# Optimization experiments

Measured on AMD Instinct MI355X. Metric: run time of the kernel, lower is better.

## Reference

```python
import jax, jax.numpy as jnp
import numpy as np

B, S, D_IN, H, G, HD = 1, 2048, 2048, 32, 8, 128
GS = H // G  # group_size = 4
D_OUT = H * HD  # 4096
EPS = 1e-6


def _rmsnorm(x, scale):
    # qwen3-compatible: compute in fp32 over last dim
    xf = x.astype(jnp.float32)
    var = jnp.mean(xf * xf, axis=-1, keepdims=True)
    return (xf * jax.lax.rsqrt(var + EPS) * scale).astype(x.dtype)


def _apply_rope(x, cos, sin):
    # x: [b, h, s, d]; cos/sin: [s, d]
    d2 = x.shape[-1] // 2
    x1, x2 = x[..., :d2], x[..., d2:]
    rotated = jnp.concatenate([-x2, x1], axis=-1)
    return (x * cos[None, None] + rotated * sin[None, None]).astype(x.dtype)


def setup_inputs() -> dict:
    key = jax.random.key(0)
    ks = jax.random.split(key, 8)
    x = jax.random.normal(ks[0], (B, S, D_IN), jnp.float32)
    mask = jnp.triu(jnp.ones((S, S), bool), k=1)  # causal: True = masked
    # RoPE tables [S, HD]
    inv_freq = 1.0 / (10000.0 ** (jnp.arange(0, HD, 2, dtype=jnp.float32) / HD))
    ang = jnp.arange(S, dtype=jnp.float32)[:, None] * inv_freq[None, :]
    ang = jnp.concatenate([ang, ang], axis=-1)
    cos, sin = jnp.cos(ang), jnp.sin(ang)
    std = 0.02
    Wq = jax.random.normal(ks[1], (D_IN, D_OUT), jnp.float32) * std
    Wk = jax.random.normal(ks[2], (D_IN, G * HD), jnp.float32) * std
    Wv = jax.random.normal(ks[3], (D_IN, G * HD), jnp.float32) * std
    Wo = jax.random.normal(ks[4], (D_OUT, D_IN), jnp.float32) * std
    q_scale = jnp.ones((HD,), jnp.float32)
    k_scale = jnp.ones((HD,), jnp.float32)
    return {"x": x, "mask": mask, "cos": cos, "sin": sin,
            "Wq": Wq, "Wk": Wk, "Wv": Wv, "Wo": Wo,
            "q_scale": q_scale, "k_scale": k_scale}


def reference(x, mask, cos, sin, Wq, Wk, Wv, Wo, q_scale, k_scale):
    b, s, _ = x.shape
    q = (x @ Wq).reshape(b, s, H, HD).transpose(0, 2, 1, 3)   # [b,H,s,hd]
    k = (x @ Wk).reshape(b, s, G, HD).transpose(0, 2, 1, 3)   # [b,G,s,hd]
    v = (x @ Wv).reshape(b, s, G, HD).transpose(0, 2, 1, 3)   # [b,G,s,hd]
    q = _rmsnorm(q, q_scale)
    k = _rmsnorm(k, k_scale)
    q = _apply_rope(q, cos[:s], sin[:s])
    k = _apply_rope(k, cos[:s], sin[:s])
    next_k, next_v = k, v  # cache (num_kv_groups heads)
    # GQA via broadcasting instead of repeat_interleave (same math)
    qg = q.reshape(b, G, GS, s, HD)
    scores = jnp.einsum('bgrsd,bgtd->bgrst', qg, k)           # [b,G,gs,s,s]
    scores = jnp.where(mask[None, None, None], -jnp.inf, scores)
    attn = jax.nn.softmax(scores / np.sqrt(HD).astype(np.float32), axis=-1)
    ctx = jnp.einsum('bgrst,bgtd->bgrsd', attn, v)            # [b,G,gs,s,hd]
    ctx = ctx.reshape(b, H, s, HD).transpose(0, 2, 1, 3).reshape(b, s, D_OUT)
    out = ctx @ Wo
    return out, next_k, next_v
```

## Files before the change

### kernel.cpp

```cpp
#include <hip/hip_runtime.h>

typedef unsigned short ushort_t;
typedef short short8 __attribute__((ext_vector_type(8)));
typedef float floatx4 __attribute__((ext_vector_type(4)));

#define S_LEN 2048
#define DIN   2048
#define NH    32
#define NG    8
#define HDIM  128
#define DOUT  4096
#define DKV   1024
#define QLD   6144

__device__ __forceinline__ float b2f(ushort_t u) {
  union { float f; unsigned u; } t; t.u = ((unsigned)u) << 16; return t.f;
}
__device__ __forceinline__ ushort_t f2b(float f) {
  union { float f; unsigned u; } t; t.f = f;
  unsigned v = t.u;
  v += 0x7FFFu + ((v >> 16) & 1u);
  return (ushort_t)(v >> 16);
}

__device__ __forceinline__ void glds16(const ushort_t* g, ushort_t* l) {
  __builtin_amdgcn_global_load_lds((const __attribute__((address_space(1))) void*)g,
                                   (__attribute__((address_space(3))) void*)l, 16, 0, 0);
}

__global__ __launch_bounds__(256) void tcastW(const float* __restrict__ Wq,
                                              const float* __restrict__ Wk,
                                              const float* __restrict__ Wv,
                                              ushort_t* __restrict__ Wt) {
  __shared__ float t[32][33];
  const int x = blockIdx.x;
  const float* W; int N, sx, drow;
  if (x < 128)      { W = Wq; N = DOUT; sx = x * 32;         drow = x * 32; }
  else if (x < 160) { W = Wk; N = DKV;  sx = (x - 128) * 32; drow = 4096 + (x - 128) * 32; }
  else              { W = Wv; N = DKV;  sx = (x - 160) * 32; drow = 5120 + (x - 160) * 32; }
  const int by = blockIdx.y * 32;
  const int tx = threadIdx.x & 31;
  const int ty = threadIdx.x >> 5;
#pragma unroll
  for (int i = 0; i < 32; i += 8)
    t[ty + i][tx] = W[(size_t)(by + ty + i) * N + sx + tx];
  __syncthreads();
#pragma unroll
  for (int i = 0; i < 32; i += 8)
    Wt[(size_t)(drow + ty + i) * DIN + by + tx] = f2b(t[tx][ty + i]);
}

__global__ __launch_bounds__(256) void tcast(const float* __restrict__ W,
                                             ushort_t* __restrict__ Wt,
                                             int N, int ldt) {
  __shared__ float t[32][33];
  const int bx = blockIdx.x * 32;
  const int by = blockIdx.y * 32;
  const int tx = threadIdx.x & 31;
  const int ty = threadIdx.x >> 5;
#pragma unroll
  for (int i = 0; i < 32; i += 8)
    t[ty + i][tx] = W[(size_t)(by + ty + i) * N + bx + tx];
  __syncthreads();
#pragma unroll
  for (int i = 0; i < 32; i += 8)
    Wt[(size_t)(bx + ty + i) * ldt + by + tx] = f2b(t[tx][ty + i]);
}

__global__ __launch_bounds__(256) void castx(const float* __restrict__ x,
                                             ushort_t* __restrict__ xb) {
  const size_t i = ((size_t)blockIdx.x * 256 + threadIdx.x) * 4;
  float4 v = *(const float4*)&x[i];
  union { int2 p; ushort_t s[4]; } w;
  w.s[0] = f2b(v.x); w.s[1] = f2b(v.y); w.s[2] = f2b(v.z); w.s[3] = f2b(v.w);
  *(int2*)&xb[i] = w.p;
}

template <int CF32, int BM>
__global__ __launch_bounds__(256) void gemm_glds(const ushort_t* __restrict__ A, int lda,
                                                 const ushort_t* __restrict__ Bt, int ldb,
                                                 void* __restrict__ Cp, int ldc, int K) {
  constexpr int MI = BM / 32;
  __shared__ __align__(16) ushort_t As[3][BM * 32];
  __shared__ __align__(16) ushort_t Bs[3][4096];
  const int tid  = threadIdx.x;
  const int m0   = blockIdx.y * BM;
  const int n0   = blockIdx.x * 128;
  const int wave = tid >> 6, lane = tid & 63;
  const int lrow = lane & 15, quad = lane >> 4;
  const int wm = (wave >> 1) * (BM / 2), wn = (wave & 1) * 64;

  floatx4 acc[MI][4];
#pragma unroll
  for (int mi = 0; mi < MI; mi++)
#pragma unroll
    for (int ni = 0; ni < 4; ni++)
#pragma unroll
      for (int j = 0; j < 4; j++) acc[mi][ni][j] = 0.0f;

  const int sc = ((tid & 3) ^ ((tid >> 3) & 3)) * 8;
  const ushort_t* ag0 = A + (size_t)(m0 + (tid >> 2)) * lda + sc;
  const ushort_t* ag1 = ag0 + (size_t)64 * lda;
  const ushort_t* bg0 = Bt + (size_t)(n0 + (tid >> 2)) * ldb + sc;
  const ushort_t* bg1 = bg0 + (size_t)64 * ldb;
  const int so = wave * 512;

  auto stage = [&](int k0, ushort_t* aB, ushort_t* bB) {
    glds16(ag0 + k0, aB + so);
    if constexpr (BM == 128) glds16(ag1 + k0, aB + 2048 + so);
    glds16(bg0 + k0, bB + so);
    glds16(bg1 + k0, bB + 2048 + so);
  };

  const int rq = (quad ^ ((lrow >> 1) & 3)) * 8;

  stage(0,  As[0], Bs[0]);
  stage(32, As[1], Bs[1]);
  stage(64, As[2], Bs[2]);

  ushort_t *a_cur = As[0], *a_n1 = As[1], *a_n2 = As[2];
  ushort_t *b_cur = Bs[0], *b_n1 = Bs[1], *b_n2 = Bs[2];

  const int NT = K >> 5;
  for (int t = 0; t < NT; t++) {
    if (t + 2 < NT) {
      if constexpr (BM == 128) asm volatile("s_waitcnt vmcnt(8)" ::: "memory");
      else                     asm volatile("s_waitcnt vmcnt(6)" ::: "memory");
    } else if (t + 1 < NT) {
      if constexpr (BM == 128) asm volatile("s_waitcnt vmcnt(4)" ::: "memory");
      else                     asm volatile("s_waitcnt vmcnt(3)" ::: "memory");
    } else {
      asm volatile("s_waitcnt vmcnt(0)" ::: "memory");
    }
    __builtin_amdgcn_s_barrier();

    short8 af[MI], bfr[4];
#pragma unroll
    for (int mi = 0; mi < MI; mi++)
      af[mi] = *(const short8*)&a_cur[(wm + mi * 16 + lrow) * 32 + rq];
#pragma unroll
    for (int ni = 0; ni < 4; ni++)
      bfr[ni] = *(const short8*)&b_cur[(wn + ni * 16 + lrow) * 32 + rq];
    asm volatile("s_waitcnt lgkmcnt(0)" ::: "memory");
    __builtin_amdgcn_s_barrier();

    if (t + 3 < NT) stage((t + 3) << 5, a_cur, b_cur);

    __builtin_amdgcn_s_setprio(1);
#pragma unroll
    for (int mi = 0; mi < MI; mi++)
#pragma unroll
      for (int ni = 0; ni < 4; ni++)
        acc[mi][ni] = __builtin_amdgcn_mfma_f32_16x16x32_bf16(af[mi], bfr[ni], acc[mi][ni], 0, 0, 0);
    __builtin_amdgcn_s_setprio(0);

    ushort_t* ta = a_cur; a_cur = a_n1; a_n1 = a_n2; a_n2 = ta;
    ushort_t* tb = b_cur; b_cur = b_n1; b_n1 = b_n2; b_n2 = tb;
  }
  asm volatile("s_waitcnt vmcnt(0)" ::: "memory");

#pragma unroll
  for (int mi = 0; mi < MI; mi++)
#pragma unroll
    for (int ni = 0; ni < 4; ni++)
#pragma unroll
      for (int i = 0; i < 4; i++) {
        const int row = m0 + wm + mi * 16 + quad * 4 + i;
        const int col = n0 + wn + ni * 16 + lrow;
        if (CF32) ((float*)Cp)[(size_t)row * ldc + col] = acc[mi][ni][i];
        else      ((ushort_t*)Cp)[(size_t)row * ldc + col] = f2b(acc[mi][ni][i]);
      }
}

__global__ __launch_bounds__(256, 2) void gemm_o(const ushort_t* __restrict__ A, int lda,
                                                 const ushort_t* __restrict__ Bt, int ldb,
                                                 float* __restrict__ C, int ldc, int K) {
  __shared__ __align__(16) ushort_t As[3][64 * 64];
  __shared__ __align__(16) ushort_t Bs[3][128 * 64];
  const int tid  = threadIdx.x;
  const int m0   = blockIdx.y * 64;
  const int n0   = blockIdx.x * 128;
  const int wave = tid >> 6, lane = tid & 63;
  const int lrow = lane & 15, quad = lane >> 4;
  const int wm = (wave >> 1) * 32, wn = (wave & 1) * 64;

  floatx4 acc[2][4];
#pragma unroll
  for (int mi = 0; mi < 2; mi++)
#pragma unroll
    for (int ni = 0; ni < 4; ni++)
#pragma unroll
      for (int j = 0; j < 4; j++) acc[mi][ni][j] = 0.0f;

  const int sc = ((lane & 7) ^ ((lane >> 3) & 7)) * 8;
  const ushort_t* ag = A  + (size_t)(m0 + wave * 8 + (lane >> 3)) * lda + sc;
  const ushort_t* bg = Bt + (size_t)(n0 + wave * 8 + (lane >> 3)) * ldb + sc;

  auto stage = [&](int k0, ushort_t* aB, ushort_t* bB) {
    glds16(ag + k0,                    aB + wave * 512);
    glds16(ag + (size_t)32 * lda + k0, aB + 2048 + wave * 512);
    glds16(bg + k0,                    bB + wave * 512);
    glds16(bg + (size_t)32 * ldb + k0, bB + 2048 + wave * 512);
    glds16(bg + (size_t)64 * ldb + k0, bB + 4096 + wave * 512);
    glds16(bg + (size_t)96 * ldb + k0, bB + 6144 + wave * 512);
  };

  const int rq0 = ((quad)     ^ (lrow & 7)) * 8;
  const int rq1 = ((4 + quad) ^ (lrow & 7)) * 8;

  stage(0,   As[0], Bs[0]);
  stage(64,  As[1], Bs[1]);
  stage(128, As[2], Bs[2]);

  ushort_t *a_cur = As[0], *a_n1 = As[1], *a_n2 = As[2];
  ushort_t *b_cur = Bs[0], *b_n1 = Bs[1], *b_n2 = Bs[2];

  const int NT = K >> 6;
  for (int t = 0; t < NT; t++) {
    if (t + 2 < NT)      asm volatile("s_waitcnt vmcnt(12)" ::: "memory");
    else if (t + 1 < NT) asm volatile("s_waitcnt vmcnt(6)" ::: "memory");
    else                 asm volatile("s_waitcnt vmcnt(0)" ::: "memory");
    __builtin_amdgcn_s_barrier();

    short8 af[2][2], bfr[2][4];
#pragma unroll
    for (int mi = 0; mi < 2; mi++) {
      af[0][mi] = *(const short8*)&a_cur[(wm + mi * 16 + lrow) * 64 + rq0];
      af[1][mi] = *(const short8*)&a_cur[(wm + mi * 16 + lrow) * 64 + rq1];
    }
#pragma unroll
    for (int ni = 0; ni < 4; ni++) {
      bfr[0][ni] = *(const short8*)&b_cur[(wn + ni * 16 + lrow) * 64 + rq0];
      bfr[1][ni] = *(const short8*)&b_cur[(wn + ni * 16 + lrow) * 64 + rq1];
    }
    asm volatile("s_waitcnt lgkmcnt(0)" ::: "memory");
    __builtin_amdgcn_s_barrier();

    if (t + 3 < NT) stage((t + 3) << 6, a_cur, b_cur);

    __builtin_amdgcn_s_setprio(1);
#pragma unroll
    for (int kd = 0; kd < 2; kd++)
#pragma unroll
      for (int mi = 0; mi < 2; mi++)
#pragma unroll
        for (int ni = 0; ni < 4; ni++)
          acc[mi][ni] = __builtin_amdgcn_mfma_f32_16x16x32_bf16(af[kd][mi], bfr[kd][ni], acc[mi][ni], 0, 0, 0);
    __builtin_amdgcn_s_setprio(0);

    ushort_t* ta = a_cur; a_cur = a_n1; a_n1 = a_n2; a_n2 = ta;
    ushort_t* tb = b_cur; b_cur = b_n1; b_n1 = b_n2; b_n2 = tb;
  }
  asm volatile("s_waitcnt vmcnt(0)" ::: "memory");

#pragma unroll
  for (int mi = 0; mi < 2; mi++)
#pragma unroll
    for (int ni = 0; ni < 4; ni++)
#pragma unroll
      for (int i = 0; i < 4; i++) {
        const int row = m0 + wm + mi * 16 + quad * 4 + i;
        const int col = n0 + wn + ni * 16 + lrow;
        C[(size_t)row * ldc + col] = acc[mi][ni][i];
      }
}

__global__ __launch_bounds__(256) void norm_qk(ushort_t* __restrict__ qkv,
                                               const float* __restrict__ cosb,
                                               const float* __restrict__ sinb,
                                               const float* __restrict__ qs,
                                               const float* __restrict__ ks,
                                               ushort_t* __restrict__ kb) {
  const int idx  = blockIdx.x * 4 + (threadIdx.x >> 6);
  const int lane = threadIdx.x & 63;
  const int SH = S_LEN * NH;
  const float QSC = 0.08838834764831845f * 1.4426950408889634f;

  if (idx < SH) {
    const int s = idx >> 5, h = idx & 31;
    ushort_t* row = qkv + (size_t)s * QLD + h * HDIM;
    float x1 = b2f(row[lane]), x2 = b2f(row[lane + 64]);
    float ss = x1 * x1 + x2 * x2;
#pragma unroll
    for (int off = 1; off < 64; off <<= 1) ss += __shfl_xor(ss, off);
    const float inv = rsqrtf(ss * (1.0f / 128.0f) + 1e-6f);
    const float y1 = x1 * inv * qs[lane] * QSC;
    const float y2 = x2 * inv * qs[lane + 64] * QSC;
    const float c1 = cosb[s * HDIM + lane],      s1 = sinb[s * HDIM + lane];
    const float c2 = cosb[s * HDIM + lane + 64], s2 = sinb[s * HDIM + lane + 64];
    row[lane]      = f2b(y1 * c1 - y2 * s1);
    row[lane + 64] = f2b(y2 * c2 + y1 * s2);
  } else {
    const int j = idx - SH;
    const int s = j >> 3, g = j & 7;
    const ushort_t* row = qkv + (size_t)s * QLD + DOUT + g * HDIM;
    float x1 = b2f(row[lane]), x2 = b2f(row[lane + 64]);
    float ss = x1 * x1 + x2 * x2;
#pragma unroll
    for (int off = 1; off < 64; off <<= 1) ss += __shfl_xor(ss, off);
    const float inv = rsqrtf(ss * (1.0f / 128.0f) + 1e-6f);
    const float y1 = x1 * inv * ks[lane];
    const float y2 = x2 * inv * ks[lane + 64];
    const float c1 = cosb[s * HDIM + lane],      s1 = sinb[s * HDIM + lane];
    const float c2 = cosb[s * HDIM + lane + 64], s2 = sinb[s * HDIM + lane + 64];
    ushort_t* o = kb + ((size_t)g * S_LEN + s) * HDIM;
    o[lane]      = f2b(y1 * c1 - y2 * s1);
    o[lane + 64] = f2b(y2 * c2 + y1 * s2);
  }
}

__global__ __launch_bounds__(256) void vtrans(const ushort_t* __restrict__ qkv,
                                              ushort_t* __restrict__ vt) {
  __shared__ ushort_t t[64][65];
  const int g = blockIdx.x;
  const int s0 = blockIdx.y * 64, d0 = blockIdx.z * 64;
  const int tx = threadIdx.x & 63, ty = threadIdx.x >> 6;
#pragma unroll
  for (int i = 0; i < 64; i += 4)
    t[ty + i][tx] = qkv[(size_t)(s0 + ty + i) * QLD + DOUT + DKV + g * HDIM + d0 + tx];
  __syncthreads();
#pragma unroll
  for (int i = 0; i < 64; i += 4)
    vt[((size_t)(g * HDIM + d0 + ty + i)) * S_LEN + s0 + tx] = t[tx][ty + i];
}

__global__ __launch_bounds__(256, 2) void attn(ushort_t* QC,
                                               const ushort_t* __restrict__ Kb,
                                               const ushort_t* __restrict__ Vt) {
  __shared__ __align__(16) ushort_t Ks[2][8192];
  __shared__ __align__(16) ushort_t Vs[2][8192];
  __shared__ __align__(16) ushort_t Ps[64 * 72];
  const int h  = blockIdx.x;
  const int qt = 31 - blockIdx.y;
  const int g  = h >> 2;
  const int tid = threadIdx.x;
  const int wave = tid >> 6, lane = tid & 63;
  const int lrow = lane & 15, quad = lane >> 4;
  const ushort_t* Kg = Kb + (size_t)g * S_LEN * HDIM;
  const ushort_t* Vg = Vt + (size_t)g * HDIM * S_LEN;
  const int r0 = qt * 64;
  const int qrow0 = r0 + wave * 16;

  short8 qf[4];
#pragma unroll
  for (int kd = 0; kd < 4; kd++)
    qf[kd] = *(const short8*)&QC[(size_t)(qrow0 + lrow) * QLD + h * HDIM + kd * 32 + quad * 8];

  short8 vones;
#pragma unroll
  for (int j = 0; j < 8; j++) vones[j] = (lrow == 0) ? (short)0x3F80 : (short)0;

  floatx4 ctx[8], ctxl;
#pragma unroll
  for (int nd = 0; nd < 8; nd++)
#pragma unroll
    for (int j = 0; j < 4; j++) ctx[nd][j] = 0.0f;
#pragma unroll
  for (int j = 0; j < 4; j++) ctxl[j] = 0.0f;

  const int swz = ((lane & 3) ^ ((lane >> 3) & 3)) * 8;
  const ushort_t* kgl = Kg + (size_t)(wave * 16 + (lane >> 2)) * HDIM + swz;
  const ushort_t* vgl = Vg + (size_t)(wave * 32 + (lane >> 2)) * S_LEN + swz;

  auto stageKV = [&](int t0, int b) {
#pragma unroll
    for (int i = 0; i < 4; i++)
      glds16(kgl + (size_t)t0 * HDIM + i * 32, &Ks[b][i * 2048 + wave * 512]);
#pragma unroll
    for (int i = 0; i < 4; i++)
      glds16(vgl + (size_t)((i >> 1) * 16) * S_LEN + t0 + (i & 1) * 32,
             &Vs[b][(i & 1) * 4096 + (wave * 32 + (i >> 1) * 16) * 32]);
  };

  const int rq = (quad ^ ((lrow >> 1) & 3)) * 8;

  stageKV(0, 0);
  if (r0 > 0) stageKV(64, 1);

  int buf = 0;
  for (int t0 = 0; t0 <= r0; t0 += 64) {
    if (t0 < r0) asm volatile("s_waitcnt vmcnt(8)" ::: "memory");
    else         asm volatile("s_waitcnt vmcnt(0)" ::: "memory");
    __builtin_amdgcn_s_barrier();
    const ushort_t* Kc = Ks[buf];
    const ushort_t* Vc = Vs[buf];

    floatx4 sacc[4];
#pragma unroll
    for (int ni = 0; ni < 4; ni++)
#pragma unroll
      for (int j = 0; j < 4; j++) sacc[ni][j] = 0.0f;
    __builtin_amdgcn_s_setprio(1);
#pragma unroll
    for (int kd = 0; kd < 4; kd++) {
      short8 kf[4];
#pragma unroll
      for (int ni = 0; ni < 4; ni++)
        kf[ni] = *(const short8*)&Kc[kd * 2048 + (ni * 16 + lrow) * 32 + rq];
#pragma unroll
      for (int ni = 0; ni < 4; ni++)
        sacc[ni] = __builtin_amdgcn_mfma_f32_16x16x32_bf16(qf[kd], kf[ni], sacc[ni], 0, 0, 0);
    }
    __builtin_amdgcn_s_setprio(0);

    const bool diag = (t0 == r0);
#pragma unroll
    for (int ni = 0; ni < 4; ni++)
#pragma unroll
      for (int i = 0; i < 4; i++) {
        float sv = sacc[ni][i];
        if (diag && (t0 + ni * 16 + lrow > qrow0 + quad * 4 + i)) sv = -1e30f;
        sacc[ni][i] = exp2f(sv - 17.0f);
      }

#pragma unroll
    for (int ni = 0; ni < 4; ni++)
#pragma unroll
      for (int i = 0; i < 4; i++)
        Ps[(wave * 16 + quad * 4 + i) * 72 + ni * 16 + lrow] = f2b(sacc[ni][i]);
    asm volatile("s_waitcnt lgkmcnt(0)" ::: "memory");

    __builtin_amdgcn_s_setprio(1);
#pragma unroll
    for (int kt = 0; kt < 2; kt++) {
      const short8 pf = *(const short8*)&Ps[(wave * 16 + lrow) * 72 + kt * 32 + quad * 8];
      ctxl = __builtin_amdgcn_mfma_f32_16x16x32_bf16(pf, vones, ctxl, 0, 0, 0);
#pragma unroll
      for (int nd = 0; nd < 8; nd++) {
        const short8 vf = *(const short8*)&Vc[kt * 4096 + (nd * 16 + lrow) * 32 + rq];
        ctx[nd] = __builtin_amdgcn_mfma_f32_16x16x32_bf16(pf, vf, ctx[nd], 0, 0, 0);
      }
    }
    __builtin_amdgcn_s_setprio(0);

    asm volatile("s_waitcnt lgkmcnt(0)" ::: "memory");
    __builtin_amdgcn_s_barrier();
    if (t0 + 128 <= r0) stageKV(t0 + 128, buf);
    buf ^= 1;
  }

  float invl[4];
#pragma unroll
  for (int i = 0; i < 4; i++) invl[i] = 1.0f / __shfl(ctxl[i], lane & 48);

  asm volatile("s_waitcnt vmcnt(0)" ::: "memory");
  __syncthreads();
  ushort_t* Es = (wave < 2) ? Ks[0] : Vs[0];
  const int eb = (wave & 1) * 16;
#pragma unroll
  for (int i = 0; i < 4; i++)
#pragma unroll
    for (int nd = 0; nd < 8; nd++)
      Es[(eb + quad * 4 + i) * 136 + nd * 16 + lrow] = f2b(ctx[nd][i] * invl[i]);
  asm volatile("s_waitcnt lgkmcnt(0)" ::: "memory");
  const int erow = lane >> 4;
  const int ecol = (lane & 15) * 8;
#pragma unroll
  for (int rr = 0; rr < 4; rr++) {
    int4 v = *(const int4*)&Es[(eb + rr * 4 + erow) * 136 + ecol];
    *(int4*)&QC[(size_t)(r0 + wave * 16 + rr * 4 + erow) * QLD + h * HDIM + ecol] = v;
  }
}

__global__ __launch_bounds__(256) void fin(const ushort_t* __restrict__ kb,
                                           const ushort_t* __restrict__ qkv,
                                           float* __restrict__ nk,
                                           float* __restrict__ nv) {
  const int bx = blockIdx.x;
  if (bx < 1024) {
    const size_t e = ((size_t)bx * 256 + threadIdx.x) * 8;
    union { int4 v; ushort_t s[8]; } u;
    u.v = *(const int4*)&kb[e];
#pragma unroll
    for (int j = 0; j < 8; j++) nk[e + j] = b2f(u.s[j]);
  } else {
    const int s = bx - 1024;
    const int g = threadIdx.x >> 5, d4 = (threadIdx.x & 31) * 4;
    union { short4 v; ushort_t s[4]; } u;
    u.v = *(const short4*)&qkv[(size_t)s * QLD + DOUT + DKV + g * HDIM + d4];
    float4 o;
    o.x = b2f(u.s[0]); o.y = b2f(u.s[1]); o.z = b2f(u.s[2]); o.w = b2f(u.s[3]);
    *(float4*)&nv[((size_t)g * S_LEN + s) * HDIM + d4] = o;
  }
}

extern "C" void kernel_launch(void* const* d_in, const int* in_sizes, int n_in,
                              void* d_out, int out_size, void* d_ws, size_t ws_size,
                              hipStream_t stream) {
  const float* x    = (const float*)d_in[0];
  const float* cosb = (const float*)d_in[2];
  const float* sinb = (const float*)d_in[3];
  const float* Wq   = (const float*)d_in[4];
  const float* Wk   = (const float*)d_in[5];
  const float* Wv   = (const float*)d_in[6];
  const float* Wo   = (const float*)d_in[7];
  const float* qs   = (const float*)d_in[8];
  const float* ks   = (const float*)d_in[9];

  float* outf = (float*)d_out;
  float* nkf  = outf + (size_t)S_LEN * DIN;
  float* nvf  = nkf + (size_t)NG * S_LEN * HDIM;

  const size_t MiB = 1024 * 1024;
  ushort_t* WallT = (ushort_t*)d_out;
  ushort_t* xb    = (ushort_t*)((char*)d_out + 24 * MiB);
  ushort_t* WoT   = (ushort_t*)((char*)d_out + 16 * MiB);
  ushort_t* vt    = (ushort_t*)d_out;
  ushort_t* qkv   = (ushort_t*)d_ws;
  ushort_t* kb    = (ushort_t*)((char*)d_ws + 24 * MiB);

  tcastW<<<dim3(192, 64), 256, 0, stream>>>(Wq, Wk, Wv, WallT);
  castx<<<4096, 256, 0, stream>>>(x, xb);

  gemm_glds<0, 128><<<dim3(48, 16), 256, 0, stream>>>(xb, DIN, WallT, DIN, qkv, QLD, DIN);

  tcast<<<dim3(64, 128), 256, 0, stream>>>(Wo, WoT, DIN, DOUT);

  norm_qk<<<(S_LEN * NH + S_LEN * NG) / 4, 256, 0, stream>>>(qkv, cosb, sinb, qs, ks, kb);

  vtrans<<<dim3(NG, S_LEN / 64, HDIM / 64), 256, 0, stream>>>(qkv, vt);

  attn<<<dim3(NH, 32), 256, 0, stream>>>(qkv, kb, vt);

  gemm_o<<<dim3(16, 32), 256, 0, stream>>>(qkv, QLD, WoT, DOUT, outf, DIN, DOUT);

  fin<<<3072, 256, 0, stream>>>(kb, qkv, nkf, nvf);
}
```

Measured before the change: 363.9 us.

## Pair causal query tiles per attention block to balance work and reuse K/V

Each attention block now handles two query tiles, qt=31-y and qt=y, so every block covers the same total number of causal key tiles, and the grid is halved to 32x16. Each staged K/V tile in shared memory is reused by both query tiles, which cuts global K/V traffic and evens out the triangular load imbalance. The cost is doubled accumulator registers (two ctx sets), which may lower occupancy or cause spills under launch_bounds(256,2). It also leaves only 512 blocks to spread across the GPU.

```diff
diff --git a/kernel.cpp b/kernel.cpp
--- a/kernel.cpp
+++ b/kernel.cpp
@@ -330,33 +330,36 @@
   __shared__ __align__(16) ushort_t Ks[2][8192];
   __shared__ __align__(16) ushort_t Vs[2][8192];
   __shared__ __align__(16) ushort_t Ps[64 * 72];
-  const int h  = blockIdx.x;
-  const int qt = 31 - blockIdx.y;
-  const int g  = h >> 2;
+  const int h   = blockIdx.x;
+  const int yb  = blockIdx.y;
+  const int qtA = 31 - yb;
+  const int qtB = yb;
+  const int g   = h >> 2;
   const int tid = threadIdx.x;
   const int wave = tid >> 6, lane = tid & 63;
   const int lrow = lane & 15, quad = lane >> 4;
   const ushort_t* Kg = Kb + (size_t)g * S_LEN * HDIM;
   const ushort_t* Vg = Vt + (size_t)g * HDIM * S_LEN;
-  const int r0 = qt * 64;
-  const int qrow0 = r0 + wave * 16;
-
-  short8 qf[4];
-#pragma unroll
-  for (int kd = 0; kd < 4; kd++)
-    qf[kd] = *(const short8*)&QC[(size_t)(qrow0 + lrow) * QLD + h * HDIM + kd * 32 + quad * 8];
+  const int rA = qtA * 64, rB = qtB * 64;
+
+  short8 qfA[4], qfB[4];
+#pragma unroll
+  for (int kd = 0; kd < 4; kd++) {
+    qfA[kd] = *(const short8*)&QC[(size_t)(rA + wave * 16 + lrow) * QLD + h * HDIM + kd * 32 + quad * 8];
+    qfB[kd] = *(const short8*)&QC[(size_t)(rB + wave * 16 + lrow) * QLD + h * HDIM + kd * 32 + quad * 8];
+  }
 
   short8 vones;
 #pragma unroll
   for (int j = 0; j < 8; j++) vones[j] = (lrow == 0) ? (short)0x3F80 : (short)0;
 
-  floatx4 ctx[8], ctxl;
+  floatx4 ctxA[8], ctxlA, ctxB[8], ctxlB;
 #pragma unroll
   for (int nd = 0; nd < 8; nd++)
 #pragma unroll
-    for (int j = 0; j < 4; j++) ctx[nd][j] = 0.0f;
-#pragma unroll
-  for (int j = 0; j < 4; j++) ctxl[j] = 0.0f;
+    for (int j = 0; j < 4; j++) { ctxA[nd][j] = 0.0f; ctxB[nd][j] = 0.0f; }
+#pragma unroll
+  for (int j = 0; j < 4; j++) { ctxlA[j] = 0.0f; ctxlB[j] = 0.0f; }
 
   const int swz = ((lane & 3) ^ ((lane >> 3) & 3)) * 8;
   const ushort_t* kgl = Kg + (size_t)(wave * 16 + (lane >> 2)) * HDIM + swz;
@@ -374,17 +377,9 @@
 
   const int rq = (quad ^ ((lrow >> 1) & 3)) * 8;
 
-  stageKV(0, 0);
-  if (r0 > 0) stageKV(64, 1);
-
-  int buf = 0;
-  for (int t0 = 0; t0 <= r0; t0 += 64) {
-    if (t0 < r0) asm volatile("s_waitcnt vmcnt(8)" ::: "memory");
-    else         asm volatile("s_waitcnt vmcnt(0)" ::: "memory");
-    __builtin_amdgcn_s_barrier();
-    const ushort_t* Kc = Ks[buf];
-    const ushort_t* Vc = Vs[buf];
-
+  auto qtile = [&](const short8 (&qf)[4], floatx4 (&ctx)[8], floatx4& ctxl,
+                   int r0, int t0, const ushort_t* Kc, const ushort_t* Vc) {
+    const int qrow0 = r0 + wave * 16;
     floatx4 sacc[4];
 #pragma unroll
     for (int ni = 0; ni < 4; ni++)
@@ -413,6 +408,7 @@
         sacc[ni][i] = exp2f(sv - 17.0f);
       }
 
+    asm volatile("s_waitcnt lgkmcnt(0)" ::: "memory");
 #pragma unroll
     for (int ni = 0; ni < 4; ni++)
 #pragma unroll
@@ -432,33 +428,66 @@
       }
     }
     __builtin_amdgcn_s_setprio(0);
+  };
+
+  stageKV(0, 0);
+  stageKV(64, 1);
+
+  int buf = 0;
+  for (int t = 0; t <= qtA; t++) {
+    const int t0 = t * 64;
+    if (t < qtA) asm volatile("s_waitcnt vmcnt(8)" ::: "memory");
+    else         asm volatile("s_waitcnt vmcnt(0)" ::: "memory");
+    __builtin_amdgcn_s_barrier();
+    const ushort_t* Kc = Ks[buf];
+    const ushort_t* Vc = Vs[buf];
+
+    qtile(qfA, ctxA, ctxlA, rA, t0, Kc, Vc);
+    if (t <= qtB) qtile(qfB, ctxB, ctxlB, rB, t0, Kc, Vc);
 
     asm volatile("s_waitcnt lgkmcnt(0)" ::: "memory");
     __builtin_amdgcn_s_barrier();
-    if (t0 + 128 <= r0) stageKV(t0 + 128, buf);
+    if (t + 2 <= qtA) stageKV((t + 2) * 64, buf);
     buf ^= 1;
   }
 
-  float invl[4];
-#pragma unroll
-  for (int i = 0; i < 4; i++) invl[i] = 1.0f / __shfl(ctxl[i], lane & 48);
+  float invlA[4], invlB[4];
+#pragma unroll
+  for (int i = 0; i < 4; i++) {
+    invlA[i] = 1.0f / __shfl(ctxlA[i], lane & 48);
+    invlB[i] = 1.0f / __shfl(ctxlB[i], lane & 48);
+  }
 
   asm volatile("s_waitcnt vmcnt(0)" ::: "memory");
   __syncthreads();
   ushort_t* Es = (wave < 2) ? Ks[0] : Vs[0];
   const int eb = (wave & 1) * 16;
-#pragma unroll
-  for (int i = 0; i < 4; i++)
-#pragma unroll
-    for (int nd = 0; nd < 8; nd++)
-      Es[(eb + quad * 4 + i) * 136 + nd * 16 + lrow] = f2b(ctx[nd][i] * invl[i]);
-  asm volatile("s_waitcnt lgkmcnt(0)" ::: "memory");
   const int erow = lane >> 4;
   const int ecol = (lane & 15) * 8;
+
+#pragma unroll
+  for (int i = 0; i < 4; i++)
+#pragma unroll
+    for (int nd = 0; nd < 8; nd++)
+      Es[(eb + quad * 4 + i) * 136 + nd * 16 + lrow] = f2b(ctxA[nd][i] * invlA[i]);
+  asm volatile("s_waitcnt lgkmcnt(0)" ::: "memory");
 #pragma unroll
   for (int rr = 0; rr < 4; rr++) {
     int4 v = *(const int4*)&Es[(eb + rr * 4 + erow) * 136 + ecol];
-    *(int4*)&QC[(size_t)(r0 + wave * 16 + rr * 4 + erow) * QLD + h * HDIM + ecol] = v;
+    *(int4*)&QC[(size_t)(rA + wave * 16 + rr * 4 + erow) * QLD + h * HDIM + ecol] = v;
+  }
+
+  asm volatile("s_waitcnt lgkmcnt(0)" ::: "memory");
+#pragma unroll
+  for (int i = 0; i < 4; i++)
+#pragma unroll
+    for (int nd = 0; nd < 8; nd++)
+      Es[(eb + quad * 4 + i) * 136 + nd * 16 + lrow] = f2b(ctxB[nd][i] * invlB[i]);
+  asm volatile("s_waitcnt lgkmcnt(0)" ::: "memory");
+#pragma unroll
+  for (int rr = 0; rr < 4; rr++) {
+    int4 v = *(const int4*)&Es[(eb + rr * 4 + erow) * 136 + ecol];
+    *(int4*)&QC[(size_t)(rB + wave * 16 + rr * 4 + erow) * QLD + h * HDIM + ecol] = v;
   }
 }
 
@@ -520,7 +549,7 @@
 
   vtrans<<<dim3(NG, S_LEN / 64, HDIM / 64), 256, 0, stream>>>(qkv, vt);
 
-  attn<<<dim3(NH, 32), 256, 0, stream>>>(qkv, kb, vt);
+  attn<<<dim3(NH, 16), 256, 0, stream>>>(qkv, kb, vt);
 
   gemm_o<<<dim3(16, 32), 256, 0, stream>>>(qkv, QLD, WoT, DOUT, outf, DIN, DOUT);
 
```

New measurement: 361.5 us. Within noise of the previous version (-0.7%).
